# Optimization experiments

Measured on AMD Instinct MI355X. Metric: run time of the kernel, lower is better.

The kernel has to match this reference:

```python
import jax, jax.numpy as jnp
import numpy as np

# Module config (mirrors init_kwargs)
B = 131072          # batch of trajectories
N_STATES = 16       # n_x_f + n_x_b
N_SEL = 8           # states selected per subnet (band width of Binary_mat)
N_U = 4             # inputs
N_FEAT = 64         # hidden width, neuron_list = [64, 64]
N_OUT = 16          # n_x_o, one output per subnet

# Binary_mat[i, j] = 1 iff (j - i) mod 16 < 8. The torch loop collects selected
# indices in INCREASING j order, so sort each row's selected set.
IDX = np.sort((np.arange(N_OUT)[:, None] + np.arange(N_SEL)[None, :]) % N_STATES, axis=1)  # [16, 8] int


def setup_inputs() -> dict:
    key = jax.random.key(0)
    k0, k1, k2, k3, k4, k5 = jax.random.split(key, 6)
    zin = N_SEL + N_U  # 12 = per-subnet MLP input width
    return {
        "x_f": jax.random.normal(k0, (B, 8), jnp.float32),
        "x_b": jax.random.normal(k1, (B, 8), jnp.float32),
        "u": jax.random.normal(k2, (B, N_U), jnp.float32),
        # stacked per-subnet weights (nn.Linear stores [out, in]); no biases
        "W0": jax.random.normal(k3, (N_OUT, N_FEAT, zin), jnp.float32) * 0.05,
        "W1": jax.random.normal(k4, (N_OUT, N_FEAT, N_FEAT), jnp.float32) * 0.05,
        "W2": jax.random.normal(k5, (N_OUT, 1, N_FEAT), jnp.float32) * 0.05,
    }


def reference(x_f, x_b, u, W0, W1, W2):
    # x_tilde = cat(x_f, x_b): [B, 16]
    x_tilde = jnp.concatenate([x_f, x_b], axis=-1)
    # Per-subnet gather of its selected state subset: [B, 16(sub), 8]
    x_sel = x_tilde[:, IDX]
    # Append exogenous input u to every subnet's input: [B, 16, 12]
    u_b = jnp.broadcast_to(u[:, None, :], (u.shape[0], N_OUT, N_U))
    z = jnp.concatenate([x_sel, u_b], axis=-1)
    # Grouped small MLPs (Linear+Tanh, Linear+Tanh, Linear) as batched GEMMs
    h = jnp.tanh(jnp.einsum('bsi,soi->bso', z, W0))   # [B, 16, 64]
    h = jnp.tanh(jnp.einsum('bsh,soh->bso', h, W1))   # [B, 16, 64]
    dx = jnp.einsum('bsh,soh->bso', h, W2)[..., 0]    # scatter into dx slices -> [B, 16]
    return dx
```

## Files before the change

### kernel.cpp

```cpp
#include <hip/hip_runtime.h>


#define N_STATES 16
#define CHUNK    4

typedef _Float16 f16x8  __attribute__((ext_vector_type(8)));
typedef float    f32x16 __attribute__((ext_vector_type(16)));
typedef __fp16   h2     __attribute__((ext_vector_type(2)));
typedef unsigned int u32x2 __attribute__((ext_vector_type(2)));

__device__ __forceinline__ h2 pack2(float a, float b) {
    return __builtin_amdgcn_cvt_pkrtz(a, b);
}
__device__ __forceinline__ unsigned int h2_bits(h2 v) {
    union { h2 h; unsigned int u; } x; x.h = v; return x.u;
}
__device__ __forceinline__ h2 bits_h2(unsigned int v) {
    union { unsigned int u; h2 h; } x; x.u = v; return x.h;
}
__device__ __forceinline__ f16x8 u4_to_h8(uint4 v) {
    union { uint4 u; f16x8 h; } x; x.u = v; return x.h;
}
__device__ __forceinline__ uint4 pk8(float4 a, float4 b) {
    return make_uint4(h2_bits(pack2(a.x, a.y)), h2_bits(pack2(a.z, a.w)),
                      h2_bits(pack2(b.x, b.y)), h2_bits(pack2(b.z, b.w)));
}

__device__ __forceinline__ h2 tanh_pk(h2 x) {
    const h2 hi = {(__fp16)1.25f, (__fp16)1.25f};
    const h2 lo = {(__fp16)-1.25f, (__fp16)-1.25f};
    const h2 k4 = {(__fp16)0.00598591f, (__fp16)0.00598591f};
    const h2 k3 = {(__fp16)-0.03807894f, (__fp16)-0.03807894f};
    const h2 k2 = {(__fp16)0.12576901f, (__fp16)0.12576901f};
    const h2 k1 = {(__fp16)-0.33203310f, (__fp16)-0.33203310f};
    const h2 k0 = {(__fp16)0.99998110f, (__fp16)0.99998110f};
    h2 s, p;
    asm("v_pk_max_f16 %0, %0, %3\n\t"
        "v_pk_min_f16 %0, %0, %4\n\t"
        "v_pk_mul_f16 %1, %0, %0\n\t"
        "v_pk_fma_f16 %2, %1, %5, %6\n\t"
        "v_pk_fma_f16 %2, %1, %2, %7\n\t"
        "v_pk_fma_f16 %2, %1, %2, %8\n\t"
        "v_pk_fma_f16 %2, %1, %2, %9\n\t"
        "v_pk_mul_f16 %0, %0, %2"
        : "+v"(x), "=&v"(s), "=&v"(p)
        : "v"(lo), "v"(hi), "v"(k4), "v"(k3), "v"(k2), "v"(k1), "v"(k0));
    return x;
}

__global__ __launch_bounds__(256, 4) void fans_mfma_kernel(
    const float* __restrict__ x_f, const float* __restrict__ x_b,
    const float* __restrict__ u,   const float* __restrict__ W0,
    const float* __restrict__ W1,  const float* __restrict__ W2,
    float* __restrict__ out)
{
    __shared__ __align__(16) uint4 zplA[256];
    __shared__ __align__(16) uint2 zplB[256];
    __shared__ __align__(16) uint4 sA1[8][64];
    __shared__ __align__(16) uint4 sA0[2][64];
    __shared__ __align__(16) unsigned int w2l[32];

    const int s   = blockIdx.y;
    const int tid = threadIdx.x;
    const int b0  = blockIdx.x * (256 * CHUNK);

    const int lid = tid & 63;
    const int w   = tid >> 6;
    const int n   = lid & 31;
    const int h   = lid >> 5;

    {
        const int r  = tid >> 2;
        const int kc = tid & 3;
        const float* p = W1 + s * 4096 + r * 64 + kc * 16;
        const float4 v0 = ((const float4*)p)[0];
        const float4 v1 = ((const float4*)p)[1];
        const float4 v2 = ((const float4*)p)[2];
        const float4 v3 = ((const float4*)p)[3];
        sA1[(r >> 5) * 4 + kc][(r & 31)]      = pk8(v0, v1);
        sA1[(r >> 5) * 4 + kc][32 + (r & 31)] = pk8(v2, v3);
    }
    if (tid < 128) {
        const int r  = tid >> 1;
        const int hh = tid & 1;
        const float* base = W0 + s * 768 + r * 12;
        uint4 v;
        if (hh == 0) {
            const float4 v0 = *(const float4*)(base + 0);
            const float4 v1 = *(const float4*)(base + 4);
            v = pk8(v0, v1);
        } else {
            const float4 v0 = *(const float4*)(base + 8);
            v = make_uint4(h2_bits(pack2(v0.x, v0.y)), h2_bits(pack2(v0.z, v0.w)), 0u, 0u);
        }
        sA0[r >> 5][hh * 32 + (r & 31)] = v;
    }
    if (tid < 32) {
        const float* w2s = W2 + s * 64;
        w2l[tid] = h2_bits(pack2(w2s[2 * tid], w2s[2 * tid + 1]));
    }
    __syncthreads();

    const int wrap = (s > 8) ? (s - 8) : 0;

    #pragma unroll 1
    for (int ch = 0; ch < CHUNK; ++ch) {
        const int rbase = b0 + ch * 256;

        {
            const int row = rbase + tid;
            float zs[8];
            #pragma unroll
            for (int j = 0; j < 8; ++j) {
                const int idx = (j < wrap) ? j : (s + j - wrap);
                zs[j] = (idx < 8) ? x_f[row * 8 + idx] : x_b[row * 8 + (idx - 8)];
            }
            const float4 uv = *(const float4*)(u + row * 4);
            zplA[tid] = make_uint4(h2_bits(pack2(zs[0], zs[1])), h2_bits(pack2(zs[2], zs[3])),
                                   h2_bits(pack2(zs[4], zs[5])), h2_bits(pack2(zs[6], zs[7])));
            zplB[tid] = make_uint2(h2_bits(pack2(uv.x, uv.y)), h2_bits(pack2(uv.z, uv.w)));
        }

        #pragma unroll
        for (int m = 0; m < 2; ++m) {
            const int rowb = 64 * w + 32 * m;

            unsigned int zero = 0;
            asm("" : "+v"(zero));
            const int lz = lid + (int)zero;

            f16x8 zf;
            if (h == 0) {
                zf = u4_to_h8(zplA[rowb + n]);
            } else {
                const uint2 b = zplB[rowb + n];
                zf = u4_to_h8(make_uint4(b.x, b.y, 0u, 0u));
            }

            const f32x16 z16 = {0.f,0.f,0.f,0.f,0.f,0.f,0.f,0.f,
                                0.f,0.f,0.f,0.f,0.f,0.f,0.f,0.f};
            f32x16 c2a = z16, c2b = z16;

            #pragma unroll
            for (int half = 0; half < 2; ++half) {
                const f16x8 a0f = u4_to_h8(sA0[half][lz]);
                f32x16 c1 = __builtin_amdgcn_mfma_f32_32x32x16_f16(a0f, zf, z16, 0, 0, 0);
                unsigned int t[8];
                #pragma unroll
                for (int a = 0; a < 4; ++a) {
                    t[2 * a + 0] = h2_bits(tanh_pk(pack2(c1[4 * a],     c1[4 * a + 1])));
                    t[2 * a + 1] = h2_bits(tanh_pk(pack2(c1[4 * a + 2], c1[4 * a + 3])));
                }
                __builtin_amdgcn_sched_barrier(0);
                #pragma unroll
                for (int kk = 0; kk < 2; ++kk) {
                    const int kc = 2 * half + kk;
                    const int q  = 4 * kk;
                    u32x2 r0 = __builtin_amdgcn_permlane32_swap(t[q + 0], t[q + 2], false, false);
                    u32x2 r1 = __builtin_amdgcn_permlane32_swap(t[q + 1], t[q + 3], false, false);
                    const f16x8 hb  = u4_to_h8(make_uint4(r0.x, r1.x, r0.y, r1.y));
                    const f16x8 w1a = u4_to_h8(sA1[kc][lz]);
                    const f16x8 w1b = u4_to_h8(sA1[4 + kc][lz]);
                    c2a = __builtin_amdgcn_mfma_f32_32x32x16_f16(w1a, hb, c2a, 0, 0, 0);
                    c2b = __builtin_amdgcn_mfma_f32_32x32x16_f16(w1b, hb, c2b, 0, 0, 0);
                }
                __builtin_amdgcn_sched_barrier(0);
            }

            const unsigned int* w2z = &w2l[zero];
            float p0 = 0.f, p1 = 0.f, q0 = 0.f, q1 = 0.f;
            #pragma unroll
            for (int a = 0; a < 4; ++a) {
                const int r = 4 * a;
                const uint2 wa = *(const uint2*)&w2z[4 * a + 2 * h];
                const uint2 wb = *(const uint2*)&w2z[16 + 4 * a + 2 * h];
                if (a & 1) {
                    p1 = __builtin_amdgcn_fdot2(tanh_pk(pack2(c2a[r], c2a[r + 1])), bits_h2(wa.x), p1, false);
                    p1 = __builtin_amdgcn_fdot2(tanh_pk(pack2(c2a[r + 2], c2a[r + 3])), bits_h2(wa.y), p1, false);
                    q1 = __builtin_amdgcn_fdot2(tanh_pk(pack2(c2b[r], c2b[r + 1])), bits_h2(wb.x), q1, false);
                    q1 = __builtin_amdgcn_fdot2(tanh_pk(pack2(c2b[r + 2], c2b[r + 3])), bits_h2(wb.y), q1, false);
                } else {
                    p0 = __builtin_amdgcn_fdot2(tanh_pk(pack2(c2a[r], c2a[r + 1])), bits_h2(wa.x), p0, false);
                    p0 = __builtin_amdgcn_fdot2(tanh_pk(pack2(c2a[r + 2], c2a[r + 3])), bits_h2(wa.y), p0, false);
                    q0 = __builtin_amdgcn_fdot2(tanh_pk(pack2(c2b[r], c2b[r + 1])), bits_h2(wb.x), q0, false);
                    q0 = __builtin_amdgcn_fdot2(tanh_pk(pack2(c2b[r + 2], c2b[r + 3])), bits_h2(wb.y), q0, false);
                }
            }
            float acc = (p0 + p1) + (q0 + q1);
            acc += __shfl_xor(acc, 32);

            if (lid < 32)
                out[(rbase + rowb + n) * N_STATES + s] = acc;
        }
    }
}

extern "C" void kernel_launch(void* const* d_in, const int* in_sizes, int n_in,
                              void* d_out, int out_size, void* d_ws, size_t ws_size,
                              hipStream_t stream) {
    const float* x_f = (const float*)d_in[0];
    const float* x_b = (const float*)d_in[1];
    const float* u   = (const float*)d_in[2];
    const float* W0  = (const float*)d_in[3];
    const float* W1  = (const float*)d_in[4];
    const float* W2  = (const float*)d_in[5];
    float* out = (float*)d_out;

    const int nb = in_sizes[0] / 8;
    dim3 grid(nb / (256 * CHUNK), N_STATES);
    fans_mfma_kernel<<<grid, 256, 0, stream>>>(x_f, x_b, u, W0, W1, W2, out);
}
```

Baseline: 123.8 us.

## Process two subnets per block, halving chunk count and interleaving subnet work

Each block now stages weights for two adjacent subnets and computes both for every row chunk. The number of row chunks per block is halved, so the total block count stays the same. The aim is to give the scheduler two independent MFMA/tanh chains, to reuse the x_f/x_b/u row loads across two subnets, and to write adjacent output columns together. The explicit sched_barriers are removed. In exchange, weight staging per block doubles and LDS use grows to about 32KB per block, which may limit occupancy.

Result: no change. 124.8 us (+0.8%).

```diff
diff --git a/kernel.cpp b/kernel.cpp
--- a/kernel.cpp
+++ b/kernel.cpp
@@ -2,7 +2,7 @@
 
 
 #define N_STATES 16
-#define CHUNK    4
+#define CHUNK    2
 
 typedef _Float16 f16x8  __attribute__((ext_vector_type(8)));
 typedef float    f32x16 __attribute__((ext_vector_type(16)));
@@ -54,13 +54,13 @@
     const float* __restrict__ W1,  const float* __restrict__ W2,
     float* __restrict__ out)
 {
-    __shared__ __align__(16) uint4 zplA[256];
-    __shared__ __align__(16) uint2 zplB[256];
-    __shared__ __align__(16) uint4 sA1[8][64];
-    __shared__ __align__(16) uint4 sA0[2][64];
-    __shared__ __align__(16) unsigned int w2l[32];
-
-    const int s   = blockIdx.y;
+    __shared__ __align__(16) uint4 zplA[2][256];
+    __shared__ __align__(16) uint2 zplB[2][256];
+    __shared__ __align__(16) uint4 sA1[2][8][64];
+    __shared__ __align__(16) uint4 sA0[2][2][64];
+    __shared__ __align__(16) unsigned int w2l[2][32];
+
+    const int sp  = blockIdx.y;
     const int tid = threadIdx.x;
     const int b0  = blockIdx.x * (256 * CHUNK);
 
@@ -69,128 +69,133 @@
     const int n   = lid & 31;
     const int h   = lid >> 5;
 
-    {
-        const int r  = tid >> 2;
-        const int kc = tid & 3;
-        const float* p = W1 + s * 4096 + r * 64 + kc * 16;
-        const float4 v0 = ((const float4*)p)[0];
-        const float4 v1 = ((const float4*)p)[1];
-        const float4 v2 = ((const float4*)p)[2];
-        const float4 v3 = ((const float4*)p)[3];
-        sA1[(r >> 5) * 4 + kc][(r & 31)]      = pk8(v0, v1);
-        sA1[(r >> 5) * 4 + kc][32 + (r & 31)] = pk8(v2, v3);
-    }
-    if (tid < 128) {
-        const int r  = tid >> 1;
-        const int hh = tid & 1;
-        const float* base = W0 + s * 768 + r * 12;
-        uint4 v;
-        if (hh == 0) {
-            const float4 v0 = *(const float4*)(base + 0);
-            const float4 v1 = *(const float4*)(base + 4);
-            v = pk8(v0, v1);
-        } else {
-            const float4 v0 = *(const float4*)(base + 8);
-            v = make_uint4(h2_bits(pack2(v0.x, v0.y)), h2_bits(pack2(v0.z, v0.w)), 0u, 0u);
-        }
-        sA0[r >> 5][hh * 32 + (r & 31)] = v;
-    }
-    if (tid < 32) {
-        const float* w2s = W2 + s * 64;
-        w2l[tid] = h2_bits(pack2(w2s[2 * tid], w2s[2 * tid + 1]));
+    #pragma unroll
+    for (int st = 0; st < 2; ++st) {
+        const int s = 2 * sp + st;
+        {
+            const int r  = tid >> 2;
+            const int kc = tid & 3;
+            const float* p = W1 + s * 4096 + r * 64 + kc * 16;
+            const float4 v0 = ((const float4*)p)[0];
+            const float4 v1 = ((const float4*)p)[1];
+            const float4 v2 = ((const float4*)p)[2];
+            const float4 v3 = ((const float4*)p)[3];
+            sA1[st][(r >> 5) * 4 + kc][(r & 31)]      = pk8(v0, v1);
+            sA1[st][(r >> 5) * 4 + kc][32 + (r & 31)] = pk8(v2, v3);
+        }
+        if (tid < 128) {
+            const int r  = tid >> 1;
+            const int hh = tid & 1;
+            const float* base = W0 + s * 768 + r * 12;
+            uint4 v;
+            if (hh == 0) {
+                const float4 v0 = *(const float4*)(base + 0);
+                const float4 v1 = *(const float4*)(base + 4);
+                v = pk8(v0, v1);
+            } else {
+                const float4 v0 = *(const float4*)(base + 8);
+                v = make_uint4(h2_bits(pack2(v0.x, v0.y)), h2_bits(pack2(v0.z, v0.w)), 0u, 0u);
+            }
+            sA0[st][r >> 5][hh * 32 + (r & 31)] = v;
+        }
+        if (tid < 32) {
+            const float* w2s = W2 + s * 64;
+            w2l[st][tid] = h2_bits(pack2(w2s[2 * tid], w2s[2 * tid + 1]));
+        }
     }
     __syncthreads();
-
-    const int wrap = (s > 8) ? (s - 8) : 0;
 
     #pragma unroll 1
     for (int ch = 0; ch < CHUNK; ++ch) {
         const int rbase = b0 + ch * 256;
 
-        {
-            const int row = rbase + tid;
+        #pragma unroll
+        for (int st = 0; st < 2; ++st) {
+            const int s    = 2 * sp + st;
+            const int wrap = (s > 8) ? (s - 8) : 0;
+            const int row  = rbase + tid;
             float zs[8];
             #pragma unroll
             for (int j = 0; j < 8; ++j) {
                 const int idx = (j < wrap) ? j : (s + j - wrap);
                 zs[j] = (idx < 8) ? x_f[row * 8 + idx] : x_b[row * 8 + (idx - 8)];
             }
-            const float4 uv = *(const float4*)(u + row * 4);
-            zplA[tid] = make_uint4(h2_bits(pack2(zs[0], zs[1])), h2_bits(pack2(zs[2], zs[3])),
-                                   h2_bits(pack2(zs[4], zs[5])), h2_bits(pack2(zs[6], zs[7])));
-            zplB[tid] = make_uint2(h2_bits(pack2(uv.x, uv.y)), h2_bits(pack2(uv.z, uv.w)));
+            const float4 uvv = *(const float4*)(u + row * 4);
+            zplA[st][tid] = make_uint4(h2_bits(pack2(zs[0], zs[1])), h2_bits(pack2(zs[2], zs[3])),
+                                       h2_bits(pack2(zs[4], zs[5])), h2_bits(pack2(zs[6], zs[7])));
+            zplB[st][tid] = make_uint2(h2_bits(pack2(uvv.x, uvv.y)), h2_bits(pack2(uvv.z, uvv.w)));
         }
 
         #pragma unroll
         for (int m = 0; m < 2; ++m) {
             const int rowb = 64 * w + 32 * m;
-
-            unsigned int zero = 0;
-            asm("" : "+v"(zero));
-            const int lz = lid + (int)zero;
-
-            f16x8 zf;
-            if (h == 0) {
-                zf = u4_to_h8(zplA[rowb + n]);
-            } else {
-                const uint2 b = zplB[rowb + n];
-                zf = u4_to_h8(make_uint4(b.x, b.y, 0u, 0u));
-            }
-
-            const f32x16 z16 = {0.f,0.f,0.f,0.f,0.f,0.f,0.f,0.f,
-                                0.f,0.f,0.f,0.f,0.f,0.f,0.f,0.f};
-            f32x16 c2a = z16, c2b = z16;
-
             #pragma unroll
-            for (int half = 0; half < 2; ++half) {
-                const f16x8 a0f = u4_to_h8(sA0[half][lz]);
-                f32x16 c1 = __builtin_amdgcn_mfma_f32_32x32x16_f16(a0f, zf, z16, 0, 0, 0);
-                unsigned int t[8];
+            for (int st = 0; st < 2; ++st) {
+                unsigned int zero = 0;
+                asm("" : "+v"(zero));
+                const int lz = lid + (int)zero;
+
+                f16x8 zf;
+                if (h == 0) {
+                    zf = u4_to_h8(zplA[st][rowb + n]);
+                } else {
+                    const uint2 b = zplB[st][rowb + n];
+                    zf = u4_to_h8(make_uint4(b.x, b.y, 0u, 0u));
+                }
+
+                const f32x16 z16 = {0.f,0.f,0.f,0.f,0.f,0.f,0.f,0.f,
+                                    0.f,0.f,0.f,0.f,0.f,0.f,0.f,0.f};
+                f32x16 c2a = z16, c2b = z16;
+
+                #pragma unroll
+                for (int half = 0; half < 2; ++half) {
+                    const f16x8 a0f = u4_to_h8(sA0[st][half][lz]);
+                    f32x16 c1 = __builtin_amdgcn_mfma_f32_32x32x16_f16(a0f, zf, z16, 0, 0, 0);
+                    unsigned int t[8];
+                    #pragma unroll
+                    for (int a = 0; a < 4; ++a) {
+                        t[2 * a + 0] = h2_bits(tanh_pk(pack2(c1[4 * a],     c1[4 * a + 1])));
+                        t[2 * a + 1] = h2_bits(tanh_pk(pack2(c1[4 * a + 2], c1[4 * a + 3])));
+                    }
+                    #pragma unroll
+                    for (int kk = 0; kk < 2; ++kk) {
+                        const int kc = 2 * half + kk;
+                        const int q  = 4 * kk;
+                        u32x2 r0 = __builtin_amdgcn_permlane32_swap(t[q + 0], t[q + 2], false, false);
+                        u32x2 r1 = __builtin_amdgcn_permlane32_swap(t[q + 1], t[q + 3], false, false);
+                        const f16x8 hb  = u4_to_h8(make_uint4(r0.x, r1.x, r0.y, r1.y));
+                        const f16x8 w1a = u4_to_h8(sA1[st][kc][lz]);
+                        const f16x8 w1b = u4_to_h8(sA1[st][4 + kc][lz]);
+                        c2a = __builtin_amdgcn_mfma_f32_32x32x16_f16(w1a, hb, c2a, 0, 0, 0);
+                        c2b = __builtin_amdgcn_mfma_f32_32x32x16_f16(w1b, hb, c2b, 0, 0, 0);
+                    }
+                }
+
+                const unsigned int* w2z = &w2l[st][zero];
+                float p0 = 0.f, p1 = 0.f, q0 = 0.f, q1 = 0.f;
                 #pragma unroll
                 for (int a = 0; a < 4; ++a) {
-                    t[2 * a + 0] = h2_bits(tanh_pk(pack2(c1[4 * a],     c1[4 * a + 1])));
-                    t[2 * a + 1] = h2_bits(tanh_pk(pack2(c1[4 * a + 2], c1[4 * a + 3])));
+                    const int r = 4 * a;
+                    const uint2 wa = *(const uint2*)&w2z[4 * a + 2 * h];
+                    const uint2 wb = *(const uint2*)&w2z[16 + 4 * a + 2 * h];
+                    if (a & 1) {
+                        p1 = __builtin_amdgcn_fdot2(tanh_pk(pack2(c2a[r], c2a[r + 1])), bits_h2(wa.x), p1, false);
+                        p1 = __builtin_amdgcn_fdot2(tanh_pk(pack2(c2a[r + 2], c2a[r + 3])), bits_h2(wa.y), p1, false);
+                        q1 = __builtin_amdgcn_fdot2(tanh_pk(pack2(c2b[r], c2b[r + 1])), bits_h2(wb.x), q1, false);
+                        q1 = __builtin_amdgcn_fdot2(tanh_pk(pack2(c2b[r + 2], c2b[r + 3])), bits_h2(wb.y), q1, false);
+                    } else {
+                        p0 = __builtin_amdgcn_fdot2(tanh_pk(pack2(c2a[r], c2a[r + 1])), bits_h2(wa.x), p0, false);
+                        p0 = __builtin_amdgcn_fdot2(tanh_pk(pack2(c2a[r + 2], c2a[r + 3])), bits_h2(wa.y), p0, false);
+                        q0 = __builtin_amdgcn_fdot2(tanh_pk(pack2(c2b[r], c2b[r + 1])), bits_h2(wb.x), q0, false);
+                        q0 = __builtin_amdgcn_fdot2(tanh_pk(pack2(c2b[r + 2], c2b[r + 3])), bits_h2(wb.y), q0, false);
+                    }
                 }
-                __builtin_amdgcn_sched_barrier(0);
-                #pragma unroll
-                for (int kk = 0; kk < 2; ++kk) {
-                    const int kc = 2 * half + kk;
-                    const int q  = 4 * kk;
-                    u32x2 r0 = __builtin_amdgcn_permlane32_swap(t[q + 0], t[q + 2], false, false);
-                    u32x2 r1 = __builtin_amdgcn_permlane32_swap(t[q + 1], t[q + 3], false, false);
-                    const f16x8 hb  = u4_to_h8(make_uint4(r0.x, r1.x, r0.y, r1.y));
-                    const f16x8 w1a = u4_to_h8(sA1[kc][lz]);
-                    const f16x8 w1b = u4_to_h8(sA1[4 + kc][lz]);
-                    c2a = __builtin_amdgcn_mfma_f32_32x32x16_f16(w1a, hb, c2a, 0, 0, 0);
-                    c2b = __builtin_amdgcn_mfma_f32_32x32x16_f16(w1b, hb, c2b, 0, 0, 0);
-                }
-                __builtin_amdgcn_sched_barrier(0);
+                float acc = (p0 + p1) + (q0 + q1);
+                acc += __shfl_xor(acc, 32);
+
+                if (lid < 32)
+                    out[(rbase + rowb + n) * N_STATES + 2 * sp + st] = acc;
             }
-
-            const unsigned int* w2z = &w2l[zero];
-            float p0 = 0.f, p1 = 0.f, q0 = 0.f, q1 = 0.f;
-            #pragma unroll
-            for (int a = 0; a < 4; ++a) {
-                const int r = 4 * a;
-                const uint2 wa = *(const uint2*)&w2z[4 * a + 2 * h];
-                const uint2 wb = *(const uint2*)&w2z[16 + 4 * a + 2 * h];
-                if (a & 1) {
-                    p1 = __builtin_amdgcn_fdot2(tanh_pk(pack2(c2a[r], c2a[r + 1])), bits_h2(wa.x), p1, false);
-                    p1 = __builtin_amdgcn_fdot2(tanh_pk(pack2(c2a[r + 2], c2a[r + 3])), bits_h2(wa.y), p1, false);
-                    q1 = __builtin_amdgcn_fdot2(tanh_pk(pack2(c2b[r], c2b[r + 1])), bits_h2(wb.x), q1, false);
-                    q1 = __builtin_amdgcn_fdot2(tanh_pk(pack2(c2b[r + 2], c2b[r + 3])), bits_h2(wb.y), q1, false);
-                } else {
-                    p0 = __builtin_amdgcn_fdot2(tanh_pk(pack2(c2a[r], c2a[r + 1])), bits_h2(wa.x), p0, false);
-                    p0 = __builtin_amdgcn_fdot2(tanh_pk(pack2(c2a[r + 2], c2a[r + 3])), bits_h2(wa.y), p0, false);
-                    q0 = __builtin_amdgcn_fdot2(tanh_pk(pack2(c2b[r], c2b[r + 1])), bits_h2(wb.x), q0, false);
-                    q0 = __builtin_amdgcn_fdot2(tanh_pk(pack2(c2b[r + 2], c2b[r + 3])), bits_h2(wb.y), q0, false);
-                }
-            }
-            float acc = (p0 + p1) + (q0 + q1);
-            acc += __shfl_xor(acc, 32);
-
-            if (lid < 32)
-                out[(rbase + rowb + n) * N_STATES + s] = acc;
         }
     }
 }
@@ -207,6 +212,6 @@
     float* out = (float*)d_out;
 
     const int nb = in_sizes[0] / 8;
-    dim3 grid(nb / (256 * CHUNK), N_STATES);
+    dim3 grid(nb / (256 * CHUNK), N_STATES / 2);
     fans_mfma_kernel<<<grid, 256, 0, stream>>>(x_f, x_b, u, W0, W1, W2, out);
 }
```
